# Performance work log

Measured on AMD Instinct MI355X. Metric: run time of the kernel, lower is better.

## Reference

```python
import jax, jax.numpy as jnp
import numpy as np

EPS = 1e-8

def _gn1(x, w, b):
    # GroupNorm(num_groups=1): normalize each sample over (C, T), per-channel affine.
    mean = jnp.mean(x, axis=(1, 2), keepdims=True)
    var = jnp.mean((x - mean) ** 2, axis=(1, 2), keepdims=True)
    xn = (x - mean) * jax.lax.rsqrt(var + EPS)
    return xn * w[None, :, None] + b[None, :, None]

def _film(h, e, gw, gb, bw, bb):
    # gamma/beta: Linear -> ReLU (dropout is identity in eval), broadcast over time.
    gamma = jax.nn.relu(e @ gw.T + gb)  # [B, C]
    beta = jax.nn.relu(e @ bw.T + bb)   # [B, C]
    return gamma[:, :, None] * h + beta[:, :, None]

def setup_inputs() -> dict:
    key = jax.random.key(0)
    ks = jax.random.split(key, 16)
    B, C, T = 16, 256, 16000
    s = lambda k, shape, scale: jax.random.normal(k, shape, dtype=jnp.float32) * scale
    return {
        "x": s(ks[0], (B, C, T), 1.0),
        "cue": s(ks[1], (B, 512), 1.0),
        "gn_a_w": jnp.ones((C,), jnp.float32), "gn_a_b": jnp.zeros((C,), jnp.float32),
        "gn_n_w": jnp.ones((C,), jnp.float32), "gn_n_b": jnp.zeros((C,), jnp.float32),
        "f1g_w": s(ks[2], (C, 512), 0.04), "f1g_b": jnp.zeros((C,), jnp.float32),
        "f1b_w": s(ks[3], (C, 512), 0.04), "f1b_b": jnp.zeros((C,), jnp.float32),
        "ln1_w": jnp.ones((C,), jnp.float32), "ln1_b": jnp.zeros((C,), jnp.float32),
        "conv1_w": s(ks[4], (128, C), 0.06),
        "cds_w": s(ks[5], (256, 512), 0.04),
        "f2g_w": s(ks[6], (128, 256), 0.06), "f2g_b": jnp.zeros((128,), jnp.float32),
        "f2b_w": s(ks[7], (128, 256), 0.06), "f2b_b": jnp.zeros((128,), jnp.float32),
        "ln2_w": jnp.ones((128,), jnp.float32), "ln2_b": jnp.zeros((128,), jnp.float32),
        "conv2_w": s(ks[8], (256, 128), 0.08),
    }

def reference(x, cue, gn_a_w, gn_a_b, gn_n_w, gn_n_b, f1g_w, f1g_b, f1b_w, f1b_b,
              ln1_w, ln1_b, conv1_w, cds_w, f2g_w, f2g_b, f2b_w, f2b_b,
              ln2_w, ln2_b, conv2_w):
    x = _gn1(x, gn_a_w, gn_a_b)                 # norm_audio (GroupNorm(1, C))
    x = _gn1(x, gn_n_w, gn_n_b)                 # norm (GroupNorm(1, C))
    x = _film(x, cue, f1g_w, f1g_b, f1b_w, f1b_b) + x  # film1 + residual
    x = _gn1(x, ln1_w, ln1_b)                   # layer_norm1
    x = jnp.einsum('bct,oc->bot', x, conv1_w)   # 1x1 Conv1d, no bias -> [B,128,T]
    cue2 = jax.nn.relu(cue @ cds_w.T)           # cue_down_sample2 -> [B,256]
    x = _film(x, cue2, f2g_w, f2g_b, f2b_w, f2b_b) + x  # film2 + residual
    x = _gn1(x, ln2_w, ln2_b)                   # layer_norm2
    x = jnp.einsum('bct,oc->bot', x, conv2_w)   # 1x1 Conv1d -> [B,256,T]
    return x
```

## Files before the change

kernel.cpp:

```cpp
#include <hip/hip_runtime.h>
#include <hip/hip_bf16.h>
#include <hip/hip_fp16.h>

#define T_LEN   16000
#define NB      16
#define NTT     250
#define NTB     125
#define EPSV    1e-8f

typedef _Float16 f16x8 __attribute__((ext_vector_type(8)));
typedef float    f32x4 __attribute__((ext_vector_type(4)));
typedef float    f32x4v __attribute__((ext_vector_type(4)));

__device__ __forceinline__ ushort f2h(float f) {
    _Float16 h = (_Float16)f;
    return *(ushort*)&h;
}
__device__ __forceinline__ float f4c(const float4& v, int i) {
    return i == 0 ? v.x : i == 1 ? v.y : i == 2 ? v.z : v.w;
}
__device__ __forceinline__ void gld16(const ushort* g, ushort* l) {
    __builtin_amdgcn_global_load_lds(
        (const __attribute__((address_space(1))) uint*)g,
        (__attribute__((address_space(3))) uint*)l, 16, 0, 0);
}
__device__ __forceinline__ float waveRed64(float v) {
    #pragma unroll
    for (int m = 1; m <= 32; m <<= 1) v += __shfl_xor(v, m, 64);
    return v;
}
__device__ __forceinline__ float4 ntload4(const float* p) {
    f32x4v v = __builtin_nontemporal_load((const f32x4v*)p);
    return make_float4(v[0], v[1], v[2], v[3]);
}

__global__ __launch_bounds__(256) void kP1_split(
    const float* __restrict__ x, ushort* __restrict__ Xp,
    float* __restrict__ sp, float* __restrict__ qp)
{
    const int tt = blockIdx.x, b = blockIdx.y;
    const int t0 = tt * 64;
    const int tid = threadIdx.x;
    const int j = tid & 15, cg = tid >> 4;
    __shared__ __align__(16) ushort Hs[64][264];

    #pragma unroll
    for (int p = 0; p < 4; ++p) {
        #pragma unroll
        for (int k = 0; k < 4; ++k) {
            const int c = k*64 + p*16 + cg;
            const float4 v = ntload4(x + ((size_t)(b*256 + c))*T_LEN + t0 + j*4);
            float s4 = 0.f, q4 = 0.f;
            #pragma unroll
            for (int i = 0; i < 4; ++i) {
                const float f = f4c(v, i);
                s4 += f; q4 += f*f;
                Hs[j*4 + i][c] = f2h(f);
            }
            #pragma unroll
            for (int m = 1; m <= 8; m <<= 1) {
                s4 += __shfl_xor(s4, m, 16);
                q4 += __shfl_xor(q4, m, 16);
            }
            if (j == 0) {
                sp[((size_t)b*NTT + tt)*256 + c] = s4;
                qp[((size_t)b*NTT + tt)*256 + c] = q4;
            }
        }
    }
    __syncthreads();
    ushort* dst = Xp + ((size_t)(b*NTT + tt)*4)*4096;
    #pragma unroll
    for (int k = 0; k < 8; ++k) {
        const int d  = tid + k*256;
        const int kc = d >> 9, r = d & 511;
        const int t  = r >> 3, us = r & 7;
        const int u  = us ^ (t & 7);
        *(uint4*)(dst + (size_t)d*8) = *(const uint4*)&Hs[t][kc*64 + u*8];
    }
}

__global__ __launch_bounds__(256) void kW1(
    const float* __restrict__ cue,
    const float* __restrict__ f1g_w, const float* __restrict__ f1g_b,
    const float* __restrict__ f1b_w, const float* __restrict__ f1b_b,
    const float* __restrict__ cds_w,
    float* __restrict__ G1, float* __restrict__ B1, float* __restrict__ CUE2)
{
    const int c = blockIdx.x;
    const int lane = threadIdx.x & 63, w = threadIdx.x >> 6;
    const float4 wg0 = *(const float4*)(f1g_w + c*512 + lane*8);
    const float4 wg1 = *(const float4*)(f1g_w + c*512 + lane*8 + 4);
    const float4 wb0 = *(const float4*)(f1b_w + c*512 + lane*8);
    const float4 wb1 = *(const float4*)(f1b_w + c*512 + lane*8 + 4);
    const float4 wc0 = *(const float4*)(cds_w + c*512 + lane*8);
    const float4 wc1 = *(const float4*)(cds_w + c*512 + lane*8 + 4);
    #pragma unroll
    for (int bb = 0; bb < 4; ++bb) {
        const int b = w*4 + bb;
        const float4 u0 = *(const float4*)(cue + b*512 + lane*8);
        const float4 u1 = *(const float4*)(cue + b*512 + lane*8 + 4);
        float g = 0.f, bt = 0.f, cv = 0.f;
        #pragma unroll
        for (int i = 0; i < 4; ++i) {
            g  = fmaf(f4c(u0,i), f4c(wg0,i), g);  g  = fmaf(f4c(u1,i), f4c(wg1,i), g);
            bt = fmaf(f4c(u0,i), f4c(wb0,i), bt); bt = fmaf(f4c(u1,i), f4c(wb1,i), bt);
            cv = fmaf(f4c(u0,i), f4c(wc0,i), cv); cv = fmaf(f4c(u1,i), f4c(wc1,i), cv);
        }
        g = waveRed64(g); bt = waveRed64(bt); cv = waveRed64(cv);
        if (lane == 0) {
            G1[b*256 + c]   = fmaxf(g + f1g_b[c], 0.f) + 1.f;
            B1[b*256 + c]   = fmaxf(bt + f1b_b[c], 0.f);
            CUE2[b*256 + c] = fmaxf(cv, 0.f);
        }
    }
}

__device__ __forceinline__ float blockSum256(float v, float* red)
{
    #pragma unroll
    for (int off = 32; off; off >>= 1) v += __shfl_down(v, off, 64);
    __syncthreads();
    if ((threadIdx.x & 63) == 0) red[threadIdx.x >> 6] = v;
    __syncthreads();
    return red[0] + red[1] + red[2] + red[3];
}

__global__ __launch_bounds__(256) void kB0(
    const float* __restrict__ sp, const float* __restrict__ qp,
    const float* __restrict__ gn_a_w, const float* __restrict__ gn_a_b,
    const float* __restrict__ gn_n_w, const float* __restrict__ gn_n_b,
    const float* __restrict__ G1, const float* __restrict__ B1,
    const float* __restrict__ ln1_w, const float* __restrict__ ln1_b,
    float* __restrict__ a4o, float* __restrict__ d4o)
{
    const int b = blockIdx.x;
    const int c = threadIdx.x;
    __shared__ float red[4];

    float sc = 0.f, qc = 0.f;
    for (int i = 0; i < NTT; ++i) {
        sc += sp[((size_t)b*NTT + i)*256 + c];
        qc += qp[((size_t)b*NTT + i)*256 + c];
    }

    const float Ninv = 1.f / (256.f * 16000.f);
    const float Tf = 16000.f;

    float S  = blockSum256(sc, red);
    float Q  = blockSum256(qc, red);
    float mu1 = S * Ninv;
    float var1 = Q * Ninv - mu1 * mu1;
    float r1 = rsqrtf(var1 + EPSV);
    float a1 = gn_a_w[c] * r1;
    float d1 = gn_a_b[c] - mu1 * r1 * gn_a_w[c];

    float S2 = blockSum256(a1*sc + Tf*d1, red);
    float Q2 = blockSum256(a1*a1*qc + 2.f*a1*d1*sc + Tf*d1*d1, red);
    float mu2 = S2 * Ninv;
    float var2 = Q2 * Ninv - mu2 * mu2;
    float r2 = rsqrtf(var2 + EPSV);
    float wn = gn_n_w[c];
    float a2 = wn * r2 * a1;
    float d2 = wn * r2 * (d1 - mu2) + gn_n_b[c];

    const float g1 = G1[b*256 + c];
    const float b1 = B1[b*256 + c];
    float a3 = g1 * a2;
    float d3 = g1 * d2 + b1;

    float S3 = blockSum256(a3*sc + Tf*d3, red);
    float Q3 = blockSum256(a3*a3*qc + 2.f*a3*d3*sc + Tf*d3*d3, red);
    float mu3 = S3 * Ninv;
    float var3 = Q3 * Ninv - mu3 * mu3;
    float r3 = rsqrtf(var3 + EPSV);
    float w1 = ln1_w[c];
    a4o[b*256 + c] = w1 * r3 * a3;
    d4o[b*256 + c] = w1 * r3 * (d3 - mu3) + ln1_b[c];
}

__global__ __launch_bounds__(256) void kM2(
    const float* __restrict__ CUE2,
    const float* __restrict__ f2g_w, const float* __restrict__ f2g_b,
    const float* __restrict__ f2b_w, const float* __restrict__ f2b_b,
    const float* __restrict__ conv1_w,
    const float* __restrict__ a4, const float* __restrict__ d4,
    float* __restrict__ G2, float* __restrict__ E, ushort* __restrict__ Msf)
{
    const int og = blockIdx.x, b = blockIdx.y;
    const int tid = threadIdx.x;
    __shared__ float sc2[256], sa4[256], sd4[256], sg2[16];
    sc2[tid] = CUE2[b*256 + tid];
    sa4[tid] = a4[b*256 + tid];
    sd4[tid] = d4[b*256 + tid];
    __syncthreads();

    const int oi = tid >> 4, l16 = tid & 15;
    const int o = og*16 + oi;
    float g = 0.f, bt = 0.f, ed = 0.f;
    #pragma unroll
    for (int q = 0; q < 4; ++q) {
        const int k0 = l16*16 + q*4;
        const float4 a  = *(const float4*)(f2g_w  + o*256 + k0);
        const float4 bb = *(const float4*)(f2b_w  + o*256 + k0);
        const float4 c  = *(const float4*)(conv1_w + o*256 + k0);
        const float4 u  = *(const float4*)(&sc2[k0]);
        const float4 dd = *(const float4*)(&sd4[k0]);
        #pragma unroll
        for (int i = 0; i < 4; ++i) {
            g  = fmaf(f4c(u,i),  f4c(a,i),  g);
            bt = fmaf(f4c(u,i),  f4c(bb,i), bt);
            ed = fmaf(f4c(dd,i), f4c(c,i),  ed);
        }
    }
    #pragma unroll
    for (int m = 1; m <= 8; m <<= 1) {
        g  += __shfl_xor(g, m, 16);
        bt += __shfl_xor(bt, m, 16);
        ed += __shfl_xor(ed, m, 16);
    }
    if (l16 == 0) {
        const float G2v = fmaxf(g + f2g_b[o], 0.f) + 1.f;
        const float B2v = fmaxf(bt + f2b_b[o], 0.f);
        G2[b*128 + o] = G2v;
        E[b*128 + o]  = G2v * ed + B2v;
        sg2[oi] = G2v;
    }
    __syncthreads();
    const float av = sa4[tid];
    #pragma unroll
    for (int i = 0; i < 16; ++i) {
        const int oo = og*16 + i;
        Msf[((size_t)b*128 + oo)*256 + tid] = f2h(sg2[i] * conv1_w[oo*256 + tid] * av);
    }
}

__global__ __launch_bounds__(256) void kC_gemm(
    const ushort* __restrict__ Xp, const ushort* __restrict__ Msf,
    const float* __restrict__ E,
    float* __restrict__ s2p, float* __restrict__ q2p)
{
    const int tb = blockIdx.x, b = blockIdx.y;
    const int tid = threadIdx.x, lane = tid & 63, w = tid >> 6;
    const int wo = w >> 1, wt = w & 1;
    const int sub = lane >> 4, li = lane & 15;
    const int o0 = wo * 64;
    __shared__ __align__(16) ushort Bs[2][8192];
    __shared__ float sSp[2][128], sQp[2][128];

    const ushort* src = Xp + ((size_t)(b*NTT + 2*tb)*4)*4096;
    const ushort* mp  = Msf + (size_t)b*128*256;

    f32x4 acc[4][4];
    #pragma unroll
    for (int i = 0; i < 4; ++i)
        #pragma unroll
        for (int jx = 0; jx < 4; ++jx) acc[i][jx] = (f32x4){0.f,0.f,0.f,0.f};

    #pragma unroll
    for (int jj = 0; jj < 4; ++jj) {
        const int m = w*4 + jj;
        const int ch = m >> 3, off = (m & 7)*512;
        gld16(src + (size_t)ch*16384 + off + lane*8, &Bs[0][ch*4096 + off]);
    }
    __syncthreads();
    for (int kc = 0; kc < 4; ++kc) {
        const int buf = kc & 1;
        if (kc < 3) {
            #pragma unroll
            for (int jj = 0; jj < 4; ++jj) {
                const int m = w*4 + jj;
                const int ch = m >> 3, off = (m & 7)*512;
                gld16(src + (size_t)ch*16384 + (kc+1)*4096 + off + lane*8,
                      &Bs[buf^1][ch*4096 + off]);
            }
        }
        f16x8 bfr[4][2];
        #pragma unroll
        for (int ft = 0; ft < 4; ++ft) {
            const int tl = ft*16 + li;
            #pragma unroll
            for (int ks = 0; ks < 2; ++ks) {
                const int u = (4*ks + sub) ^ (tl & 7);
                bfr[ft][ks] = *(const f16x8*)&Bs[buf][wt*4096 + tl*64 + u*8];
            }
        }
        #pragma unroll
        for (int ks = 0; ks < 2; ++ks) {
            #pragma unroll
            for (int fo = 0; fo < 4; ++fo) {
                const f16x8 a = *(const f16x8*)(mp + (size_t)(o0 + fo*16 + li)*256 + kc*64 + ks*32 + 8*sub);
                #pragma unroll
                for (int ft = 0; ft < 4; ++ft)
                    acc[fo][ft] = __builtin_amdgcn_mfma_f32_16x16x32_f16(a, bfr[ft][ks], acc[fo][ft], 0, 0, 0);
            }
        }
        __syncthreads();
    }

    #pragma unroll
    for (int fo = 0; fo < 4; ++fo) {
        #pragma unroll
        for (int r = 0; r < 4; ++r) {
            const int o = o0 + fo*16 + sub*4 + r;
            const float ev = E[b*128 + o];
            float sv = 0.f, qv = 0.f;
            #pragma unroll
            for (int ft = 0; ft < 4; ++ft) {
                const float z = acc[fo][ft][r] + ev;
                sv += z; qv += z*z;
            }
            #pragma unroll
            for (int m = 1; m <= 8; m <<= 1) {
                sv += __shfl_xor(sv, m, 64);
                qv += __shfl_xor(qv, m, 64);
            }
            if (li == 0) { sSp[wt][o] = sv; sQp[wt][o] = qv; }
        }
    }
    __syncthreads();
    if (tid < 128) {
        s2p[((size_t)b*NTB + tb)*128 + tid] = sSp[0][tid] + sSp[1][tid];
        q2p[((size_t)b*NTB + tb)*128 + tid] = sQp[0][tid] + sQp[1][tid];
    }
}

__global__ __launch_bounds__(256) void kE_gemm(
    const ushort* __restrict__ Xp, const ushort* __restrict__ Fsf,
    const float* __restrict__ h, float* __restrict__ out)
{
    const int tt = blockIdx.x, b = blockIdx.y;
    const int tid = threadIdx.x, lane = tid & 63, w = tid >> 6;
    const int sub = lane >> 4, li = lane & 15;
    const int o0 = w * 64, t0 = tt * 64;
    __shared__ __align__(16) ushort Bs[2][4096];
    __shared__ __align__(16) float Ts[4][16][68];

    const ushort* src = Xp + ((size_t)(b*NTT + tt)*4)*4096;
    const ushort* fp  = Fsf + (size_t)b*65536;

    f32x4 acc[4][4];
    #pragma unroll
    for (int i = 0; i < 4; ++i)
        #pragma unroll
        for (int jx = 0; jx < 4; ++jx) acc[i][jx] = (f32x4){0.f,0.f,0.f,0.f};

    #pragma unroll
    for (int jj = 0; jj < 2; ++jj) {
        const int m = w*2 + jj;
        gld16(src + m*512 + lane*8, &Bs[0][m*512]);
    }
    __syncthreads();
    for (int kc = 0; kc < 4; ++kc) {
        const int buf = kc & 1;
        if (kc < 3) {
            #pragma unroll
            for (int jj = 0; jj < 2; ++jj) {
                const int m = w*2 + jj;
                gld16(src + (kc+1)*4096 + m*512 + lane*8, &Bs[buf^1][m*512]);
            }
        }
        f16x8 bfr[4][2];
        #pragma unroll
        for (int ft = 0; ft < 4; ++ft) {
            const int t = ft*16 + li;
            #pragma unroll
            for (int ks = 0; ks < 2; ++ks) {
                const int u = (4*ks + sub) ^ (t & 7);
                bfr[ft][ks] = *(const f16x8*)&Bs[buf][t*64 + u*8];
            }
        }
        #pragma unroll
        for (int ks = 0; ks < 2; ++ks) {
            #pragma unroll
            for (int fo = 0; fo < 4; ++fo) {
                const f16x8 a = *(const f16x8*)(fp + (size_t)(o0 + fo*16 + li)*256 + kc*64 + ks*32 + 8*sub);
                #pragma unroll
                for (int ft = 0; ft < 4; ++ft)
                    acc[fo][ft] = __builtin_amdgcn_mfma_f32_16x16x32_f16(a, bfr[ft][ks], acc[fo][ft], 0, 0, 0);
            }
        }
        __syncthreads();
    }

    #pragma unroll
    for (int fo = 0; fo < 4; ++fo) {
        float hv[4];
        #pragma unroll
        for (int r = 0; r < 4; ++r)
            hv[r] = h[b*256 + o0 + fo*16 + sub*4 + r];
        #pragma unroll
        for (int ft = 0; ft < 4; ++ft)
            #pragma unroll
            for (int r = 0; r < 4; ++r)
                Ts[w][sub*4 + r][ft*16 + li] = acc[fo][ft][r] + hv[r];
        #pragma unroll
        for (int it = 0; it < 4; ++it) {
            const int row = it*4 + sub;
            const f32x4v v = *(const f32x4v*)&Ts[w][row][li*4];
            __builtin_nontemporal_store(v,
                (f32x4v*)(out + ((size_t)(b*256 + o0 + fo*16 + row))*T_LEN + t0 + li*4));
        }
    }
}

__global__ __launch_bounds__(128) void kD1_finalize(
    const float* __restrict__ s2p, const float* __restrict__ q2p,
    const float* __restrict__ ln2_w, const float* __restrict__ ln2_b,
    const float* __restrict__ E,
    float* __restrict__ A2, float* __restrict__ AE)
{
    const int b = blockIdx.x;
    const int o = threadIdx.x;
    float s = 0.f, qq = 0.f;
    for (int tb = 0; tb < NTB; ++tb) {
        s  += s2p[((size_t)b*NTB + tb)*128 + o];
        qq += q2p[((size_t)b*NTB + tb)*128 + o];
    }
    float S = s, Q = qq;
    #pragma unroll
    for (int off = 32; off; off >>= 1) {
        S += __shfl_down(S, off, 64);
        Q += __shfl_down(Q, off, 64);
    }
    __shared__ float rS[2], rQ[2];
    if ((o & 63) == 0) { rS[o >> 6] = S; rQ[o >> 6] = Q; }
    __syncthreads();
    const float N2inv = 1.f / (128.f * 16000.f);
    const float mu  = (rS[0] + rS[1]) * N2inv;
    const float var = (rQ[0] + rQ[1]) * N2inv - mu * mu;
    const float r = rsqrtf(var + EPSV);
    const float a2v = ln2_w[o] * r;
    const float d2v = ln2_b[o] - mu * ln2_w[o] * r;
    A2[b*128 + o] = a2v;
    AE[b*128 + o] = a2v * E[b*128 + o] + d2v;
}

__global__ __launch_bounds__(256) void kD2_buildF(
    const float* __restrict__ a4, const float* __restrict__ G2,
    const float* __restrict__ A2, const float* __restrict__ AE,
    const float* __restrict__ conv1_w, const float* __restrict__ conv2_w,
    ushort* __restrict__ Fsf, float* __restrict__ h)
{
    const int b = blockIdx.y, pg = blockIdx.x;
    const int tid = threadIdx.x;
    __shared__ float Qs[32][128];
    #pragma unroll
    for (int k = 0; k < 16; ++k) {
        const int idx = tid + k*256;
        const int p = idx >> 7, o = idx & 127;
        Qs[p][o] = conv2_w[(pg*32 + p)*128 + o] * A2[b*128 + o] * G2[b*128 + o];
    }
    __syncthreads();
    float acc[32];
    #pragma unroll
    for (int p = 0; p < 32; ++p) acc[p] = 0.f;
    for (int o = 0; o < 128; ++o) {
        const float mv = conv1_w[o*256 + tid];
        #pragma unroll
        for (int p = 0; p < 32; ++p) acc[p] = fmaf(Qs[p][o], mv, acc[p]);
    }
    const float a = a4[b*256 + tid];
    #pragma unroll
    for (int p = 0; p < 32; ++p) {
        const size_t idx = ((size_t)b*256 + pg*32 + p)*256 + tid;
        Fsf[idx] = f2h(acc[p] * a);
    }
    if (tid < 32) {
        const int p = pg*32 + tid;
        float hv = 0.f;
        for (int o = 0; o < 128; ++o)
            hv += conv2_w[p*128 + o] * AE[b*128 + o];
        h[b*256 + p] = hv;
    }
}

extern "C" void kernel_launch(void* const* d_in, const int* in_sizes, int n_in,
                              void* d_out, int out_size, void* d_ws, size_t ws_size,
                              hipStream_t stream)
{
    const float* x       = (const float*)d_in[0];
    const float* cue     = (const float*)d_in[1];
    const float* gn_a_w  = (const float*)d_in[2];
    const float* gn_a_b  = (const float*)d_in[3];
    const float* gn_n_w  = (const float*)d_in[4];
    const float* gn_n_b  = (const float*)d_in[5];
    const float* f1g_w   = (const float*)d_in[6];
    const float* f1g_b   = (const float*)d_in[7];
    const float* f1b_w   = (const float*)d_in[8];
    const float* f1b_b   = (const float*)d_in[9];
    const float* ln1_w   = (const float*)d_in[10];
    const float* ln1_b   = (const float*)d_in[11];
    const float* conv1_w = (const float*)d_in[12];
    const float* cds_w   = (const float*)d_in[13];
    const float* f2g_w   = (const float*)d_in[14];
    const float* f2g_b   = (const float*)d_in[15];
    const float* f2b_w   = (const float*)d_in[16];
    const float* f2b_b   = (const float*)d_in[17];
    const float* ln2_w   = (const float*)d_in[18];
    const float* ln2_b   = (const float*)d_in[19];
    const float* conv2_w = (const float*)d_in[20];
    float* out = (float*)d_out;

    float* ws = (float*)d_ws;
    float*  sp   = ws;
    float*  qp   = ws + 1024000;
    float*  G1   = ws + 2048000;
    float*  B1   = ws + 2052096;
    float*  CUE2 = ws + 2056192;
    float*  G2   = ws + 2060288;
    float*  a4   = ws + 2062336;
    float*  d4   = ws + 2066432;
    float*  E    = ws + 2070528;
    float*  A2   = ws + 2072576;
    float*  AE   = ws + 2074624;
    float*  h    = ws + 2076672;
    float*  s2p  = ws + 2080768;
    float*  q2p  = ws + 2336768;
    ushort* Msf  = (ushort*)(ws + 2592768);
    ushort* Fsf  = (ushort*)(ws + 2854912);
    ushort* Xp   = (ushort*)(ws + 3379200);

    kP1_split<<<dim3(NTT, NB), 256, 0, stream>>>(x, Xp, sp, qp);

    kW1<<<256, 256, 0, stream>>>(cue, f1g_w, f1g_b, f1b_w, f1b_b, cds_w,
                                 G1, B1, CUE2);

    kB0<<<NB, 256, 0, stream>>>(sp, qp, gn_a_w, gn_a_b, gn_n_w, gn_n_b,
                                G1, B1, ln1_w, ln1_b, a4, d4);

    kM2<<<dim3(8, NB), 256, 0, stream>>>(CUE2, f2g_w, f2g_b, f2b_w, f2b_b,
                                         conv1_w, a4, d4, G2, E, Msf);

    kC_gemm<<<dim3(NTB, NB), 256, 0, stream>>>(Xp, Msf, E, s2p, q2p);

    kD1_finalize<<<NB, 128, 0, stream>>>(s2p, q2p, ln2_w, ln2_b, E, A2, AE);

    kD2_buildF<<<dim3(8, NB), 256, 0, stream>>>(a4, G2, A2, AE,
                                                conv1_w, conv2_w, Fsf, h);

    kE_gemm<<<dim3(NTT, NB), 256, 0, stream>>>(Xp, Fsf, h, out);
}
```

Measured before the change: 322.1 us.

## Fuse small stat kernels and widen output GEMM tiles to 128 time steps

Merges the GroupNorm finalize kernel with the FiLM2/Msf build kernel into one per-batch kernel, and folds the layer_norm2 finalize into the F-matrix build kernel, removing two launches and their global round-trips. The output GEMM now processes 128 time steps per block (8 MFMA column tiles, double-buffered 16 KB LDS). It reuses that LDS buffer as the staging area for the output transpose. The fused per-batch kernel runs only 16 blocks serially over 8 output groups, so it may become slower than the parallel version. The larger accumulator raises register pressure in the output GEMM.

```diff
diff --git a/kernel.cpp b/kernel.cpp
--- a/kernel.cpp
+++ b/kernel.cpp
@@ -10,7 +10,6 @@
 
 typedef _Float16 f16x8 __attribute__((ext_vector_type(8)));
 typedef float    f32x4 __attribute__((ext_vector_type(4)));
-typedef float    f32x4v __attribute__((ext_vector_type(4)));
 
 __device__ __forceinline__ ushort f2h(float f) {
     _Float16 h = (_Float16)f;
@@ -30,7 +29,7 @@
     return v;
 }
 __device__ __forceinline__ float4 ntload4(const float* p) {
-    f32x4v v = __builtin_nontemporal_load((const f32x4v*)p);
+    f32x4 v = __builtin_nontemporal_load((const f32x4*)p);
     return make_float4(v[0], v[1], v[2], v[3]);
 }
 
@@ -126,17 +125,23 @@
     return red[0] + red[1] + red[2] + red[3];
 }
 
-__global__ __launch_bounds__(256) void kB0(
+__global__ __launch_bounds__(256) void kBM(
     const float* __restrict__ sp, const float* __restrict__ qp,
     const float* __restrict__ gn_a_w, const float* __restrict__ gn_a_b,
     const float* __restrict__ gn_n_w, const float* __restrict__ gn_n_b,
     const float* __restrict__ G1, const float* __restrict__ B1,
     const float* __restrict__ ln1_w, const float* __restrict__ ln1_b,
-    float* __restrict__ a4o, float* __restrict__ d4o)
+    const float* __restrict__ CUE2,
+    const float* __restrict__ f2g_w, const float* __restrict__ f2g_b,
+    const float* __restrict__ f2b_w, const float* __restrict__ f2b_b,
+    const float* __restrict__ conv1_w,
+    float* __restrict__ a4o, float* __restrict__ G2,
+    float* __restrict__ E, ushort* __restrict__ Msf)
 {
     const int b = blockIdx.x;
     const int c = threadIdx.x;
     __shared__ float red[4];
+    __shared__ float sa4[256], sd4[256], sc2[256], sg2[16];
 
     float sc = 0.f, qc = 0.f;
     for (int i = 0; i < NTT; ++i) {
@@ -175,63 +180,54 @@
     float var3 = Q3 * Ninv - mu3 * mu3;
     float r3 = rsqrtf(var3 + EPSV);
     float w1 = ln1_w[c];
-    a4o[b*256 + c] = w1 * r3 * a3;
-    d4o[b*256 + c] = w1 * r3 * (d3 - mu3) + ln1_b[c];
-}
-
-__global__ __launch_bounds__(256) void kM2(
-    const float* __restrict__ CUE2,
-    const float* __restrict__ f2g_w, const float* __restrict__ f2g_b,
-    const float* __restrict__ f2b_w, const float* __restrict__ f2b_b,
-    const float* __restrict__ conv1_w,
-    const float* __restrict__ a4, const float* __restrict__ d4,
-    float* __restrict__ G2, float* __restrict__ E, ushort* __restrict__ Msf)
-{
-    const int og = blockIdx.x, b = blockIdx.y;
-    const int tid = threadIdx.x;
-    __shared__ float sc2[256], sa4[256], sd4[256], sg2[16];
-    sc2[tid] = CUE2[b*256 + tid];
-    sa4[tid] = a4[b*256 + tid];
-    sd4[tid] = d4[b*256 + tid];
-    __syncthreads();
-
-    const int oi = tid >> 4, l16 = tid & 15;
-    const int o = og*16 + oi;
-    float g = 0.f, bt = 0.f, ed = 0.f;
-    #pragma unroll
-    for (int q = 0; q < 4; ++q) {
-        const int k0 = l16*16 + q*4;
-        const float4 a  = *(const float4*)(f2g_w  + o*256 + k0);
-        const float4 bb = *(const float4*)(f2b_w  + o*256 + k0);
-        const float4 c  = *(const float4*)(conv1_w + o*256 + k0);
-        const float4 u  = *(const float4*)(&sc2[k0]);
-        const float4 dd = *(const float4*)(&sd4[k0]);
-        #pragma unroll
-        for (int i = 0; i < 4; ++i) {
-            g  = fmaf(f4c(u,i),  f4c(a,i),  g);
-            bt = fmaf(f4c(u,i),  f4c(bb,i), bt);
-            ed = fmaf(f4c(dd,i), f4c(c,i),  ed);
-        }
-    }
-    #pragma unroll
-    for (int m = 1; m <= 8; m <<= 1) {
-        g  += __shfl_xor(g, m, 16);
-        bt += __shfl_xor(bt, m, 16);
-        ed += __shfl_xor(ed, m, 16);
-    }
-    if (l16 == 0) {
-        const float G2v = fmaxf(g + f2g_b[o], 0.f) + 1.f;
-        const float B2v = fmaxf(bt + f2b_b[o], 0.f);
-        G2[b*128 + o] = G2v;
-        E[b*128 + o]  = G2v * ed + B2v;
-        sg2[oi] = G2v;
-    }
-    __syncthreads();
-    const float av = sa4[tid];
-    #pragma unroll
-    for (int i = 0; i < 16; ++i) {
-        const int oo = og*16 + i;
-        Msf[((size_t)b*128 + oo)*256 + tid] = f2h(sg2[i] * conv1_w[oo*256 + tid] * av);
+    const float a4v = w1 * r3 * a3;
+    const float d4v = w1 * r3 * (d3 - mu3) + ln1_b[c];
+    sa4[c] = a4v;
+    sd4[c] = d4v;
+    a4o[b*256 + c] = a4v;
+    sc2[c] = CUE2[b*256 + c];
+    __syncthreads();
+
+    const int oi = c >> 4, l16 = c & 15;
+    for (int og = 0; og < 8; ++og) {
+        const int o = og*16 + oi;
+        float g = 0.f, bt = 0.f, ed = 0.f;
+        #pragma unroll
+        for (int q = 0; q < 4; ++q) {
+            const int k0 = l16*16 + q*4;
+            const float4 a  = *(const float4*)(f2g_w  + o*256 + k0);
+            const float4 bb = *(const float4*)(f2b_w  + o*256 + k0);
+            const float4 cc = *(const float4*)(conv1_w + o*256 + k0);
+            const float4 u  = *(const float4*)(&sc2[k0]);
+            const float4 dd = *(const float4*)(&sd4[k0]);
+            #pragma unroll
+            for (int i = 0; i < 4; ++i) {
+                g  = fmaf(f4c(u,i),  f4c(a,i),  g);
+                bt = fmaf(f4c(u,i),  f4c(bb,i), bt);
+                ed = fmaf(f4c(dd,i), f4c(cc,i), ed);
+            }
+        }
+        #pragma unroll
+        for (int m = 1; m <= 8; m <<= 1) {
+            g  += __shfl_xor(g, m, 16);
+            bt += __shfl_xor(bt, m, 16);
+            ed += __shfl_xor(ed, m, 16);
+        }
+        if (l16 == 0) {
+            const float G2v = fmaxf(g + f2g_b[o], 0.f) + 1.f;
+            const float B2v = fmaxf(bt + f2b_b[o], 0.f);
+            G2[b*128 + o] = G2v;
+            E[b*128 + o]  = G2v * ed + B2v;
+            sg2[oi] = G2v;
+        }
+        __syncthreads();
+        const float av = sa4[c];
+        #pragma unroll
+        for (int i = 0; i < 16; ++i) {
+            const int oo = og*16 + i;
+            Msf[((size_t)b*128 + oo)*256 + c] = f2h(sg2[i] * conv1_w[oo*256 + c] * av);
+        }
+        __syncthreads();
     }
 }
 
@@ -325,131 +321,52 @@
     }
 }
 
-__global__ __launch_bounds__(256) void kE_gemm(
-    const ushort* __restrict__ Xp, const ushort* __restrict__ Fsf,
-    const float* __restrict__ h, float* __restrict__ out)
-{
-    const int tt = blockIdx.x, b = blockIdx.y;
-    const int tid = threadIdx.x, lane = tid & 63, w = tid >> 6;
-    const int sub = lane >> 4, li = lane & 15;
-    const int o0 = w * 64, t0 = tt * 64;
-    __shared__ __align__(16) ushort Bs[2][4096];
-    __shared__ __align__(16) float Ts[4][16][68];
-
-    const ushort* src = Xp + ((size_t)(b*NTT + tt)*4)*4096;
-    const ushort* fp  = Fsf + (size_t)b*65536;
-
-    f32x4 acc[4][4];
-    #pragma unroll
-    for (int i = 0; i < 4; ++i)
-        #pragma unroll
-        for (int jx = 0; jx < 4; ++jx) acc[i][jx] = (f32x4){0.f,0.f,0.f,0.f};
-
-    #pragma unroll
-    for (int jj = 0; jj < 2; ++jj) {
-        const int m = w*2 + jj;
-        gld16(src + m*512 + lane*8, &Bs[0][m*512]);
-    }
-    __syncthreads();
-    for (int kc = 0; kc < 4; ++kc) {
-        const int buf = kc & 1;
-        if (kc < 3) {
-            #pragma unroll
-            for (int jj = 0; jj < 2; ++jj) {
-                const int m = w*2 + jj;
-                gld16(src + (kc+1)*4096 + m*512 + lane*8, &Bs[buf^1][m*512]);
-            }
-        }
-        f16x8 bfr[4][2];
-        #pragma unroll
-        for (int ft = 0; ft < 4; ++ft) {
-            const int t = ft*16 + li;
-            #pragma unroll
-            for (int ks = 0; ks < 2; ++ks) {
-                const int u = (4*ks + sub) ^ (t & 7);
-                bfr[ft][ks] = *(const f16x8*)&Bs[buf][t*64 + u*8];
-            }
-        }
-        #pragma unroll
-        for (int ks = 0; ks < 2; ++ks) {
-            #pragma unroll
-            for (int fo = 0; fo < 4; ++fo) {
-                const f16x8 a = *(const f16x8*)(fp + (size_t)(o0 + fo*16 + li)*256 + kc*64 + ks*32 + 8*sub);
-                #pragma unroll
-                for (int ft = 0; ft < 4; ++ft)
-                    acc[fo][ft] = __builtin_amdgcn_mfma_f32_16x16x32_f16(a, bfr[ft][ks], acc[fo][ft], 0, 0, 0);
-            }
-        }
-        __syncthreads();
-    }
-
-    #pragma unroll
-    for (int fo = 0; fo < 4; ++fo) {
-        float hv[4];
-        #pragma unroll
-        for (int r = 0; r < 4; ++r)
-            hv[r] = h[b*256 + o0 + fo*16 + sub*4 + r];
-        #pragma unroll
-        for (int ft = 0; ft < 4; ++ft)
-            #pragma unroll
-            for (int r = 0; r < 4; ++r)
-                Ts[w][sub*4 + r][ft*16 + li] = acc[fo][ft][r] + hv[r];
-        #pragma unroll
-        for (int it = 0; it < 4; ++it) {
-            const int row = it*4 + sub;
-            const f32x4v v = *(const f32x4v*)&Ts[w][row][li*4];
-            __builtin_nontemporal_store(v,
-                (f32x4v*)(out + ((size_t)(b*256 + o0 + fo*16 + row))*T_LEN + t0 + li*4));
-        }
-    }
-}
-
-__global__ __launch_bounds__(128) void kD1_finalize(
+__global__ __launch_bounds__(256) void kD2_buildF(
     const float* __restrict__ s2p, const float* __restrict__ q2p,
     const float* __restrict__ ln2_w, const float* __restrict__ ln2_b,
-    const float* __restrict__ E,
-    float* __restrict__ A2, float* __restrict__ AE)
-{
-    const int b = blockIdx.x;
-    const int o = threadIdx.x;
+    const float* __restrict__ Ev,
+    const float* __restrict__ a4, const float* __restrict__ G2,
+    const float* __restrict__ conv1_w, const float* __restrict__ conv2_w,
+    ushort* __restrict__ Fsf, float* __restrict__ h)
+{
+    const int b = blockIdx.y, pg = blockIdx.x;
+    const int tid = threadIdx.x;
+    __shared__ float Qs[32][128];
+    __shared__ float sA2[128], sAE[128];
+    __shared__ float rS[2], rQ[2];
+
     float s = 0.f, qq = 0.f;
-    for (int tb = 0; tb < NTB; ++tb) {
-        s  += s2p[((size_t)b*NTB + tb)*128 + o];
-        qq += q2p[((size_t)b*NTB + tb)*128 + o];
-    }
-    float S = s, Q = qq;
-    #pragma unroll
-    for (int off = 32; off; off >>= 1) {
-        S += __shfl_down(S, off, 64);
-        Q += __shfl_down(Q, off, 64);
-    }
-    __shared__ float rS[2], rQ[2];
-    if ((o & 63) == 0) { rS[o >> 6] = S; rQ[o >> 6] = Q; }
+    if (tid < 128) {
+        for (int tb = 0; tb < NTB; ++tb) {
+            s  += s2p[((size_t)b*NTB + tb)*128 + tid];
+            qq += q2p[((size_t)b*NTB + tb)*128 + tid];
+        }
+        float S = s, Q = qq;
+        #pragma unroll
+        for (int off = 32; off; off >>= 1) {
+            S += __shfl_down(S, off, 64);
+            Q += __shfl_down(Q, off, 64);
+        }
+        if ((tid & 63) == 0) { rS[tid >> 6] = S; rQ[tid >> 6] = Q; }
+    }
     __syncthreads();
     const float N2inv = 1.f / (128.f * 16000.f);
     const float mu  = (rS[0] + rS[1]) * N2inv;
     const float var = (rQ[0] + rQ[1]) * N2inv - mu * mu;
     const float r = rsqrtf(var + EPSV);
-    const float a2v = ln2_w[o] * r;
-    const float d2v = ln2_b[o] - mu * ln2_w[o] * r;
-    A2[b*128 + o] = a2v;
-    AE[b*128 + o] = a2v * E[b*128 + o] + d2v;
-}
-
-__global__ __launch_bounds__(256) void kD2_buildF(
-    const float* __restrict__ a4, const float* __restrict__ G2,
-    const float* __restrict__ A2, const float* __restrict__ AE,
-    const float* __restrict__ conv1_w, const float* __restrict__ conv2_w,
-    ushort* __restrict__ Fsf, float* __restrict__ h)
-{
-    const int b = blockIdx.y, pg = blockIdx.x;
-    const int tid = threadIdx.x;
-    __shared__ float Qs[32][128];
+    if (tid < 128) {
+        const float a2v = ln2_w[tid] * r;
+        const float d2v = ln2_b[tid] - mu * ln2_w[tid] * r;
+        sA2[tid] = a2v;
+        sAE[tid] = a2v * Ev[b*128 + tid] + d2v;
+    }
+    __syncthreads();
+
     #pragma unroll
     for (int k = 0; k < 16; ++k) {
         const int idx = tid + k*256;
         const int p = idx >> 7, o = idx & 127;
-        Qs[p][o] = conv2_w[(pg*32 + p)*128 + o] * A2[b*128 + o] * G2[b*128 + o];
+        Qs[p][o] = conv2_w[(pg*32 + p)*128 + o] * sA2[o] * G2[b*128 + o];
     }
     __syncthreads();
     float acc[32];
@@ -470,8 +387,96 @@
         const int p = pg*32 + tid;
         float hv = 0.f;
         for (int o = 0; o < 128; ++o)
-            hv += conv2_w[p*128 + o] * AE[b*128 + o];
+            hv += conv2_w[p*128 + o] * sAE[o];
         h[b*256 + p] = hv;
+    }
+}
+
+__global__ __launch_bounds__(256) void kE_gemm(
+    const ushort* __restrict__ Xp, const ushort* __restrict__ Fsf,
+    const float* __restrict__ h, float* __restrict__ out)
+{
+    const int tt = blockIdx.x, b = blockIdx.y;
+    const int tid = threadIdx.x, lane = tid & 63, w = tid >> 6;
+    const int sub = lane >> 4, li = lane & 15;
+    const int o0 = w * 64, t0 = tt * 128;
+    __shared__ __align__(16) ushort Bs[2][8192];
+
+    const ushort* fp = Fsf + (size_t)b*65536;
+    const size_t cbase = ((size_t)b*NTT + 2*tt)*4;
+
+    f32x4 acc[4][8];
+    #pragma unroll
+    for (int i = 0; i < 4; ++i)
+        #pragma unroll
+        for (int jx = 0; jx < 8; ++jx) acc[i][jx] = (f32x4){0.f,0.f,0.f,0.f};
+
+    #pragma unroll
+    for (int jj = 0; jj < 4; ++jj) {
+        const int m = w*4 + jj;
+        const int half = m >> 3, mm = m & 7;
+        gld16(Xp + (cbase + half*4 + 0)*4096 + mm*512 + lane*8,
+              &Bs[0][half*4096 + mm*512]);
+    }
+    __syncthreads();
+    for (int kc = 0; kc < 4; ++kc) {
+        const int buf = kc & 1;
+        if (kc < 3) {
+            #pragma unroll
+            for (int jj = 0; jj < 4; ++jj) {
+                const int m = w*4 + jj;
+                const int half = m >> 3, mm = m & 7;
+                gld16(Xp + (cbase + half*4 + (kc+1))*4096 + mm*512 + lane*8,
+                      &Bs[buf^1][half*4096 + mm*512]);
+            }
+        }
+        #pragma unroll
+        for (int ks = 0; ks < 2; ++ks) {
+            f16x8 bfr[8];
+            #pragma unroll
+            for (int ft = 0; ft < 8; ++ft) {
+                const int t = ft*16 + li;
+                const int half = t >> 6, tl = t & 63;
+                const int u = (4*ks + sub) ^ (tl & 7);
+                bfr[ft] = *(const f16x8*)&Bs[buf][half*4096 + tl*64 + u*8];
+            }
+            #pragma unroll
+            for (int fo = 0; fo < 4; ++fo) {
+                const f16x8 a = *(const f16x8*)(fp + (size_t)(o0 + fo*16 + li)*256 + kc*64 + ks*32 + 8*sub);
+                #pragma unroll
+                for (int ft = 0; ft < 8; ++ft)
+                    acc[fo][ft] = __builtin_amdgcn_mfma_f32_16x16x32_f16(a, bfr[ft], acc[fo][ft], 0, 0, 0);
+            }
+        }
+        __syncthreads();
+    }
+
+    float* Ts = (float*)(&Bs[0][0]) + w * (16*68);
+    #pragma unroll
+    for (int fo = 0; fo < 4; ++fo) {
+        float hv[4];
+        #pragma unroll
+        for (int r = 0; r < 4; ++r)
+            hv[r] = h[b*256 + o0 + fo*16 + sub*4 + r];
+        #pragma unroll
+        for (int ph = 0; ph < 2; ++ph) {
+            #pragma unroll
+            for (int f4 = 0; f4 < 4; ++f4) {
+                const int ft = ph*4 + f4;
+                #pragma unroll
+                for (int r = 0; r < 4; ++r)
+                    Ts[(sub*4 + r)*68 + f4*16 + li] = acc[fo][ft][r] + hv[r];
+            }
+            #pragma unroll
+            for (int it = 0; it < 4; ++it) {
+                const int row = it*4 + sub;
+                const f32x4 v = *(const f32x4*)&Ts[row*68 + li*4];
+                __builtin_nontemporal_store(v,
+                    (f32x4*)(out + ((size_t)(b*256 + o0 + fo*16 + row))*T_LEN
+                             + t0 + ph*64 + li*4));
+            }
+            asm volatile("s_waitcnt lgkmcnt(0)" ::: "memory");
+        }
     }
 }
 
@@ -510,34 +515,29 @@
     float*  CUE2 = ws + 2056192;
     float*  G2   = ws + 2060288;
     float*  a4   = ws + 2062336;
-    float*  d4   = ws + 2066432;
-    float*  E    = ws + 2070528;
-    float*  A2   = ws + 2072576;
-    float*  AE   = ws + 2074624;
-    float*  h    = ws + 2076672;
-    float*  s2p  = ws + 2080768;
-    float*  q2p  = ws + 2336768;
-    ushort* Msf  = (ushort*)(ws + 2592768);
-    ushort* Fsf  = (ushort*)(ws + 2854912);
-    ushort* Xp   = (ushort*)(ws + 3379200);
+    float*  E    = ws + 2066432;
+    float*  h    = ws + 2068480;
+    float*  s2p  = ws + 2072576;
+    float*  q2p  = ws + 2328576;
+    ushort* Msf  = (ushort*)(ws + 2584576);
+    ushort* Fsf  = (ushort*)(ws + 2846720);
+    ushort* Xp   = (ushort*)(ws + 3371008);
 
     kP1_split<<<dim3(NTT, NB), 256, 0, stream>>>(x, Xp, sp, qp);
 
     kW1<<<256, 256, 0, stream>>>(cue, f1g_w, f1g_b, f1b_w, f1b_b, cds_w,
                                  G1, B1, CUE2);
 
-    kB0<<<NB, 256, 0, stream>>>(sp, qp, gn_a_w, gn_a_b, gn_n_w, gn_n_b,
-                                G1, B1, ln1_w, ln1_b, a4, d4);
-
-    kM2<<<dim3(8, NB), 256, 0, stream>>>(CUE2, f2g_w, f2g_b, f2b_w, f2b_b,
-                                         conv1_w, a4, d4, G2, E, Msf);
+    kBM<<<NB, 256, 0, stream>>>(sp, qp, gn_a_w, gn_a_b, gn_n_w, gn_n_b,
+                                G1, B1, ln1_w, ln1_b, CUE2,
+                                f2g_w, f2g_b, f2b_w, f2b_b, conv1_w,
+                                a4, G2, E, Msf);
 
     kC_gemm<<<dim3(NTB, NB), 256, 0, stream>>>(Xp, Msf, E, s2p, q2p);
 
-    kD1_finalize<<<NB, 128, 0, stream>>>(s2p, q2p, ln2_w, ln2_b, E, A2, AE);
-
-    kD2_buildF<<<dim3(8, NB), 256, 0, stream>>>(a4, G2, A2, AE,
-                                                conv1_w, conv2_w, Fsf, h);
-
-    kE_gemm<<<dim3(NTT, NB), 256, 0, stream>>>(Xp, Fsf, h, out);
-}
+    kD2_buildF<<<dim3(8, NB), 256, 0, stream>>>(s2p, q2p, ln2_w, ln2_b, E,
+                                                a4, G2, conv1_w, conv2_w,
+                                                Fsf, h);
+
+    kE_gemm<<<dim3(NTB, NB), 256, 0, stream>>>(Xp, Fsf, h, out);
+}
```

Result: faster. 313.7 us (-2.6%).
